# Optimization experiments

Hardware: AMD Instinct MI355X
Metric: run time of the kernel (lower is better)

Reference implementation:

```python
import jax, jax.numpy as jnp
import numpy as np

B = 8192          # number of nodes / batch
DEG = 32          # neighbors per node (fixed-degree instance of the ragged pattern)
E = B * DEG       # total neighbor rows
D = 256           # embedding_dim
A = 128           # attn_dim
ACT = 512         # action_dim
SLOPE = 0.2       # leakyrelu slope


def setup_inputs() -> dict:
    key = jax.random.key(0)
    ks = jax.random.split(key, 12)
    inp = {
        "state": jax.random.normal(ks[0], (B, 2 * D), jnp.float32),
        "now_embedding": jax.random.normal(ks[1], (B, D), jnp.float32),
        "neigh": jax.random.normal(ks[2], (E, D), jnp.float32),
        "seg_ids": jnp.repeat(jnp.arange(B, dtype=jnp.int32), DEG),  # sorted segment ids
        # attention projection Linear(D, A)
        "attn_w": jax.random.normal(ks[3], (D, A), jnp.float32) * (1.0 / np.sqrt(D)),
        "attn_b": jnp.zeros((A,), jnp.float32),
        # attn_weight Linear(2A, 1)
        "aw_w": jax.random.normal(ks[4], (2 * A, 1), jnp.float32) * (1.0 / np.sqrt(2 * A)),
        "aw_b": jnp.zeros((1,), jnp.float32),
        # MLP head
        "w1": jax.random.normal(ks[5], (3 * D, 512), jnp.float32) * (1.0 / np.sqrt(3 * D)),
        "b1": jnp.zeros((512,), jnp.float32),
        "w2": jax.random.normal(ks[6], (512, 1024), jnp.float32) * (1.0 / np.sqrt(512)),
        "b2": jnp.zeros((1024,), jnp.float32),
        "w3": jax.random.normal(ks[7], (1024, ACT), jnp.float32) * (1.0 / np.sqrt(1024)),
        "b3": jnp.zeros((ACT,), jnp.float32),
    }
    return inp


def reference(state, now_embedding, neigh, seg_ids, attn_w, attn_b, aw_w, aw_b,
              w1, b1, w2, b2, w3, b3):
    # project center and neighbor embeddings to attn space
    now_proj = now_embedding @ attn_w + attn_b          # [B, A]
    nb_proj = neigh @ attn_w + attn_b                   # [E, A]
    # attn_weight applied to concat([now_proj[seg], nb_proj]) == split matvec
    w_now, w_nb = aw_w[:A, 0], aw_w[A:, 0]              # [A], [A]
    scores = (now_proj @ w_now)[seg_ids] + nb_proj @ w_nb + aw_b[0]   # [E]
    scores = jnp.where(scores >= 0, scores, SLOPE * scores)           # LeakyReLU(0.2)
    # per-segment (per-node) softmax over neighbors
    seg_max = jax.ops.segment_max(scores, seg_ids, num_segments=B)
    e = jnp.exp(scores - seg_max[seg_ids])
    seg_sum = jax.ops.segment_sum(e, seg_ids, num_segments=B)
    alpha = e / seg_sum[seg_ids]                        # [E]
    # weighted aggregation of raw neighbor embeddings
    agg = jax.ops.segment_sum(alpha[:, None] * neigh, seg_ids, num_segments=B)  # [B, D]
    # MLP head (dropout prob = 0 -> identity)
    out = jnp.concatenate([state, agg], axis=1)         # [B, 3D]
    out = jax.nn.relu(out @ w1 + b1)
    out = jax.nn.relu(out @ w2 + b2)
    out = out @ w3 + b3
    return jax.nn.softmax(out, axis=-1)
```

## Files before the change

kernel.cpp:

```cpp
#include <hip/hip_runtime.h>
#include <hip/hip_bf16.h>

#define B_SEG  8192
#define DEG    32
#define D_DIM  256
#define TWO_D  512
#define ACTD   512
#define SLOPE  0.2f

typedef __attribute__((ext_vector_type(8))) short bf16x8;
typedef __attribute__((ext_vector_type(4))) float f32x4;

#define OFF_VNOW  ((size_t)0)
#define OFF_VNB   ((size_t)1024)
#define OFF_CNST  ((size_t)2048)
#define OFF_W1T   ((size_t)4096)
#define OFF_W2T   (OFF_W1T + (size_t)768*512*2)
#define OFF_W3T   (OFF_W2T + (size_t)512*1024*2)
#define OFF_X1    (OFF_W3T + (size_t)1024*512*2)
#define OFF_X2    (OFF_X1 + (size_t)B_SEG*768*2)
#define OFF_X3    (OFF_X2 + (size_t)B_SEG*512*2)

typedef const unsigned int __attribute__((address_space(1)))* gas_ptr;
typedef unsigned int __attribute__((address_space(3)))* las_ptr;

__device__ __forceinline__ void gload_lds16(const void* g, void* l) {
    __builtin_amdgcn_global_load_lds((gas_ptr)g, (las_ptr)l, 16, 0, 0);
}

__global__ __launch_bounds__(256) void prep_vec(
        const float* __restrict__ attn_w, const float* __restrict__ attn_b,
        const float* __restrict__ aw_w, const float* __restrict__ aw_b,
        float* __restrict__ vnow, float* __restrict__ vnb, float* __restrict__ cnst) {
    const int d = threadIdx.x;
    float s0 = 0.f, s1 = 0.f;
    for (int a = 0; a < 128; ++a) {
        const float w = attn_w[d * 128 + a];
        s0 = fmaf(w, aw_w[a], s0);
        s1 = fmaf(w, aw_w[128 + a], s1);
    }
    vnow[d] = s0;
    vnb[d]  = s1;
    if (d == 0) {
        float c = aw_b[0];
        for (int a = 0; a < 128; ++a) c = fmaf(attn_b[a], aw_w[a] + aw_w[128 + a], c);
        cnst[0] = c;
    }
}

__global__ __launch_bounds__(256) void attn_tr(
        const float* __restrict__ state, const float* __restrict__ now_emb,
        const float* __restrict__ neigh, const float* __restrict__ vnow,
        const float* __restrict__ vnb, const float* __restrict__ cnst,
        __hip_bfloat16* __restrict__ X1,
        const float* __restrict__ w1, const float* __restrict__ w2,
        const float* __restrict__ w3,
        __hip_bfloat16* __restrict__ w1T, __hip_bfloat16* __restrict__ w2T,
        __hip_bfloat16* __restrict__ w3T) {
    __shared__ __align__(16) float smem[1088];
    const int bid = blockIdx.x;

    if (bid >= B_SEG) {
        int pb = bid - B_SEG;
        const float* src;
        __hip_bfloat16* dst;
        int K, N;
        if (pb < 384)      { src = w1; dst = w1T; K = 768;  N = 512;  }
        else if (pb < 896) { pb -= 384; src = w2; dst = w2T; K = 512;  N = 1024; }
        else               { pb -= 896; src = w3; dst = w3T; K = 1024; N = 512;  }
        const int tk = K >> 5;
        const int bk = (pb % tk) * 32;
        const int bn = (pb / tk) * 32;
        float (*tile)[33] = (float(*)[33])smem;
        const int tx = threadIdx.x & 31;
        const int ty = threadIdx.x >> 5;
#pragma unroll
        for (int i = 0; i < 32; i += 8)
            tile[ty + i][tx] = src[(size_t)(bk + ty + i) * N + (bn + tx)];
        __syncthreads();
#pragma unroll
        for (int i = 0; i < 32; i += 8)
            dst[(size_t)(bn + ty + i) * K + (bk + tx)] = __float2bfloat16(tile[tx][ty + i]);
        return;
    }

    const int b    = bid;
    const int tid  = threadIdx.x;
    const int lane = tid & 63;
    const int w    = tid >> 6;
    const int l4   = lane * 4;

    float* s_part  = smem;
    float* s_score = smem + 1024;
    float* s_now   = smem + 1056;

    const float4 vb = *(const float4*)&vnb[l4];
    float4 nv[8];
#pragma unroll
    for (int i = 0; i < 8; ++i) {
        const int e = w * 8 + i;
        nv[i] = *(const float4*)&neigh[((size_t)b * DEG + e) * D_DIM + l4];
        float p = nv[i].x * vb.x + nv[i].y * vb.y + nv[i].z * vb.z + nv[i].w * vb.w;
#pragma unroll
        for (int off = 32; off; off >>= 1) p += __shfl_xor(p, off);
        if (lane == 0) s_score[e] = p;
    }
    if (w == 0) {
        const float4 va = *(const float4*)&vnow[l4];
        const float4 ne = *(const float4*)&now_emb[(size_t)b * D_DIM + l4];
        float p = ne.x * va.x + ne.y * va.y + ne.z * va.z + ne.w * va.w;
#pragma unroll
        for (int off = 32; off; off >>= 1) p += __shfl_xor(p, off);
        if (lane == 0) s_now[0] = p + cnst[0];
    }
    __syncthreads();

    if (w == 0) {
        float s = (lane < DEG) ? (s_score[lane] + s_now[0]) : -3.4e38f;
        s = (s >= 0.f) ? s : SLOPE * s;
        float m = s;
#pragma unroll
        for (int off = 32; off; off >>= 1) m = fmaxf(m, __shfl_xor(m, off));
        const float e = (lane < DEG) ? expf(s - m) : 0.f;
        float t = e;
#pragma unroll
        for (int off = 32; off; off >>= 1) t += __shfl_xor(t, off);
        if (lane < DEG) s_score[lane] = e / t;
    }
    __syncthreads();

    float4 part = {0.f, 0.f, 0.f, 0.f};
#pragma unroll
    for (int i = 0; i < 8; ++i) {
        const float al = s_score[w * 8 + i];
        part.x = fmaf(al, nv[i].x, part.x);
        part.y = fmaf(al, nv[i].y, part.y);
        part.z = fmaf(al, nv[i].z, part.z);
        part.w = fmaf(al, nv[i].w, part.w);
    }
    *(float4*)&s_part[w * D_DIM + l4] = part;
    __syncthreads();

    const float a = s_part[tid] + s_part[D_DIM + tid] + s_part[2 * D_DIM + tid] +
                    s_part[3 * D_DIM + tid];

    __hip_bfloat16* xrow = X1 + (size_t)b * 768;
    xrow[512 + tid] = __float2bfloat16(a);
    const float2 st = *(const float2*)&state[(size_t)b * TWO_D + 2 * tid];
    __hip_bfloat162 h;
    h.x = __float2bfloat16(st.x);
    h.y = __float2bfloat16(st.y);
    *(__hip_bfloat162*)&xrow[2 * tid] = h;
}

template <int RELU, int OUTF32>
__global__ __launch_bounds__(256) void gemm_mfma(
        const __hip_bfloat16* __restrict__ A, const __hip_bfloat16* __restrict__ BT,
        const float* __restrict__ bias, void* __restrict__ Cout, int N, int K) {
    __shared__ __hip_bfloat16 sA[64 * 32];
    __shared__ __hip_bfloat16 sB[128 * 32];

    const int tid  = threadIdx.x;
    const int lane = tid & 63;
    const int wv   = tid >> 6;
    const int wr   = wv >> 1;
    const int wc   = wv & 1;
    const size_t mBase = (size_t)blockIdx.x * 64;
    const size_t nBase = (size_t)blockIdx.y * 128;

    f32x4 acc[2][4];
#pragma unroll
    for (int r = 0; r < 2; ++r)
#pragma unroll
        for (int c = 0; c < 4; ++c) acc[r][c] = (f32x4){0.f, 0.f, 0.f, 0.f};

    const int srow = tid >> 2;
    const int sseg = tid & 3;
    const __hip_bfloat16* gA  = A  + (mBase + srow) * (size_t)K + sseg * 8;
    const __hip_bfloat16* gB0 = BT + (nBase + srow) * (size_t)K + sseg * 8;
    const __hip_bfloat16* gB1 = gB0 + (size_t)64 * K;
    char* ldsA = (char*)&sA[0] + tid * 16;
    char* ldsB = (char*)&sB[0] + tid * 16;

    const int fr  = lane & 15;
    const int fkb = (lane >> 4) * 16;

    for (int k0 = 0; k0 < K; k0 += 32) {
        gload_lds16(gA + k0, ldsA);
        gload_lds16(gB0 + k0, ldsB);
        gload_lds16(gB1 + k0, ldsB + 4096);
        __syncthreads();

        bf16x8 aF[2], bF[4];
#pragma unroll
        for (int r = 0; r < 2; ++r)
            aF[r] = *(const bf16x8*)((const char*)sA + (wr * 32 + r * 16 + fr) * 64 + fkb);
#pragma unroll
        for (int c = 0; c < 4; ++c)
            bF[c] = *(const bf16x8*)((const char*)sB + (wc * 64 + c * 16 + fr) * 64 + fkb);
#pragma unroll
        for (int r = 0; r < 2; ++r)
#pragma unroll
            for (int c = 0; c < 4; ++c)
                acc[r][c] = __builtin_amdgcn_mfma_f32_16x16x32_bf16(aF[r], bF[c], acc[r][c], 0, 0, 0);
        __syncthreads();
    }

    const int fq = lane >> 4;
#pragma unroll
    for (int r = 0; r < 2; ++r) {
#pragma unroll
        for (int c = 0; c < 4; ++c) {
            const size_t col = nBase + wc * 64 + c * 16 + fr;
            const float bcol = bias[col];
#pragma unroll
            for (int q = 0; q < 4; ++q) {
                const size_t row = mBase + wr * 32 + r * 16 + fq * 4 + q;
                float v = acc[r][c][q] + bcol;
                if (RELU) v = fmaxf(v, 0.f);
                if (OUTF32) ((float*)Cout)[row * N + col] = v;
                else ((__hip_bfloat16*)Cout)[row * N + col] = __float2bfloat16(v);
            }
        }
    }
}

__global__ __launch_bounds__(512) void gemm3_softmax(
        const __hip_bfloat16* __restrict__ A, const __hip_bfloat16* __restrict__ BT,
        const float* __restrict__ bias, float* __restrict__ out) {
    constexpr int K = 1024;
    constexpr int N = 512;
    __shared__ __hip_bfloat16 sA[32 * 32];
    __shared__ __hip_bfloat16 sB[512 * 32];
    __shared__ float s_max[8][32];
    __shared__ float s_sum[8][32];
    __shared__ float s_gmax[32];
    __shared__ float s_ginv[32];

    const int tid  = threadIdx.x;
    const int lane = tid & 63;
    const int wv   = tid >> 6;
    const size_t mBase = (size_t)blockIdx.x * 32;

    f32x4 acc[2][4];
#pragma unroll
    for (int r = 0; r < 2; ++r)
#pragma unroll
        for (int c = 0; c < 4; ++c) acc[r][c] = (f32x4){0.f, 0.f, 0.f, 0.f};

    const __hip_bfloat16* gA = A + (mBase + (tid >> 2)) * (size_t)K + (tid & 3) * 8;
    char* ldsA = (char*)&sA[0] + tid * 16;
    const __hip_bfloat16* gB[4];
    char* ldsB[4];
#pragma unroll
    for (int i = 0; i < 4; ++i) {
        const int s = tid + i * 512;
        gB[i]   = BT + (size_t)(s >> 2) * K + (s & 3) * 8;
        ldsB[i] = (char*)&sB[0] + s * 16;
    }

    const int fr  = lane & 15;
    const int fkb = (lane >> 4) * 16;

    for (int k0 = 0; k0 < K; k0 += 32) {
        if (tid < 128) gload_lds16(gA + k0, ldsA);
#pragma unroll
        for (int i = 0; i < 4; ++i) gload_lds16(gB[i] + k0, ldsB[i]);
        __syncthreads();

        bf16x8 aF[2], bF[4];
#pragma unroll
        for (int r = 0; r < 2; ++r)
            aF[r] = *(const bf16x8*)((const char*)sA + (r * 16 + fr) * 64 + fkb);
#pragma unroll
        for (int c = 0; c < 4; ++c)
            bF[c] = *(const bf16x8*)((const char*)sB + (wv * 64 + c * 16 + fr) * 64 + fkb);
#pragma unroll
        for (int r = 0; r < 2; ++r)
#pragma unroll
            for (int c = 0; c < 4; ++c)
                acc[r][c] = __builtin_amdgcn_mfma_f32_16x16x32_bf16(aF[r], bF[c], acc[r][c], 0, 0, 0);
        __syncthreads();
    }

    const int fq = lane >> 4;
    float bcol[4];
#pragma unroll
    for (int c = 0; c < 4; ++c) bcol[c] = bias[wv * 64 + c * 16 + fr];

    float rm[2][4];
#pragma unroll
    for (int r = 0; r < 2; ++r)
#pragma unroll
        for (int q = 0; q < 4; ++q) {
            float m = -3.4e38f;
#pragma unroll
            for (int c = 0; c < 4; ++c) {
                acc[r][c][q] += bcol[c];
                m = fmaxf(m, acc[r][c][q]);
            }
#pragma unroll
            for (int off = 8; off; off >>= 1) m = fmaxf(m, __shfl_xor(m, off));
            rm[r][q] = m;
        }
    if (fr == 0) {
#pragma unroll
        for (int r = 0; r < 2; ++r)
#pragma unroll
            for (int q = 0; q < 4; ++q) s_max[wv][r * 16 + fq * 4 + q] = rm[r][q];
    }
    __syncthreads();
    if (tid < 32) {
        float m = s_max[0][tid];
#pragma unroll
        for (int w2_ = 1; w2_ < 8; ++w2_) m = fmaxf(m, s_max[w2_][tid]);
        s_gmax[tid] = m;
    }
    __syncthreads();

    float rs[2][4];
#pragma unroll
    for (int r = 0; r < 2; ++r)
#pragma unroll
        for (int q = 0; q < 4; ++q) {
            const float gm = s_gmax[r * 16 + fq * 4 + q];
            float s = 0.f;
#pragma unroll
            for (int c = 0; c < 4; ++c) {
                acc[r][c][q] = expf(acc[r][c][q] - gm);
                s += acc[r][c][q];
            }
#pragma unroll
            for (int off = 8; off; off >>= 1) s += __shfl_xor(s, off);
            rs[r][q] = s;
        }
    if (fr == 0) {
#pragma unroll
        for (int r = 0; r < 2; ++r)
#pragma unroll
            for (int q = 0; q < 4; ++q) s_sum[wv][r * 16 + fq * 4 + q] = rs[r][q];
    }
    __syncthreads();
    if (tid < 32) {
        float t = s_sum[0][tid];
#pragma unroll
        for (int w2_ = 1; w2_ < 8; ++w2_) t += s_sum[w2_][tid];
        s_ginv[tid] = 1.f / t;
    }
    __syncthreads();

#pragma unroll
    for (int r = 0; r < 2; ++r)
#pragma unroll
        for (int q = 0; q < 4; ++q) {
            const float inv = s_ginv[r * 16 + fq * 4 + q];
            const size_t row = mBase + r * 16 + fq * 4 + q;
#pragma unroll
            for (int c = 0; c < 4; ++c)
                out[row * N + wv * 64 + c * 16 + fr] = acc[r][c][q] * inv;
        }
}

extern "C" void kernel_launch(void* const* d_in, const int* in_sizes, int n_in,
                              void* d_out, int out_size, void* d_ws, size_t ws_size,
                              hipStream_t stream) {
    const float* state   = (const float*)d_in[0];
    const float* now_emb = (const float*)d_in[1];
    const float* neigh   = (const float*)d_in[2];
    const float* attn_w  = (const float*)d_in[4];
    const float* attn_b  = (const float*)d_in[5];
    const float* aw_w    = (const float*)d_in[6];
    const float* aw_b    = (const float*)d_in[7];
    const float* w1      = (const float*)d_in[8];
    const float* b1      = (const float*)d_in[9];
    const float* w2      = (const float*)d_in[10];
    const float* b2      = (const float*)d_in[11];
    const float* w3      = (const float*)d_in[12];
    const float* b3      = (const float*)d_in[13];
    float* out = (float*)d_out;

    char* ws = (char*)d_ws;
    float*          vnow = (float*)(ws + OFF_VNOW);
    float*          vnb  = (float*)(ws + OFF_VNB);
    float*          cnst = (float*)(ws + OFF_CNST);
    __hip_bfloat16* w1T  = (__hip_bfloat16*)(ws + OFF_W1T);
    __hip_bfloat16* w2T  = (__hip_bfloat16*)(ws + OFF_W2T);
    __hip_bfloat16* w3T  = (__hip_bfloat16*)(ws + OFF_W3T);
    __hip_bfloat16* X1   = (__hip_bfloat16*)(ws + OFF_X1);
    __hip_bfloat16* X2   = (__hip_bfloat16*)(ws + OFF_X2);
    __hip_bfloat16* X3   = (__hip_bfloat16*)(ws + OFF_X3);

    prep_vec<<<1, 256, 0, stream>>>(attn_w, attn_b, aw_w, aw_b, vnow, vnb, cnst);
    attn_tr<<<B_SEG + 1408, 256, 0, stream>>>(state, now_emb, neigh, vnow, vnb, cnst, X1,
                                              w1, w2, w3, w1T, w2T, w3T);
    gemm_mfma<1, 0><<<dim3(128, 4), 256, 0, stream>>>(X1, w1T, b1, (void*)X2, 512, 768);
    gemm_mfma<1, 0><<<dim3(128, 8), 256, 0, stream>>>(X2, w2T, b2, (void*)X3, 1024, 512);
    gemm3_softmax<<<256, 512, 0, stream>>>(X3, w3T, b3, out);
}
```

Before: 149.5 us.

## Double-buffer MLP GEMMs with swizzled LDS and move weight transpose into prep kernel

The two ReLU GEMMs now use a 64-wide K tile with two LDS buffers and an XOR-swizzled layout, so the next tile's global-to-LDS loads are issued while the current tile feeds the MFMAs, and LDS bank conflicts are reduced. The final GEMM+softmax kernel gets the same double buffering. The weight transpose blocks move out of the attention kernel into the prep kernel, which also absorbs the vector precompute, giving attention a simpler launch. The cost is more LDS per block, which may lower occupancy, and the prep kernel's serial block 0 now shares a launch with the transposes.

New measurement: 143.1 us. -4.3%, faster.

```diff
diff --git a/kernel.cpp b/kernel.cpp
--- a/kernel.cpp
+++ b/kernel.cpp
@@ -28,71 +28,68 @@
     __builtin_amdgcn_global_load_lds((gas_ptr)g, (las_ptr)l, 16, 0, 0);
 }
 
-__global__ __launch_bounds__(256) void prep_vec(
+__global__ __launch_bounds__(256) void prep_all(
         const float* __restrict__ attn_w, const float* __restrict__ attn_b,
         const float* __restrict__ aw_w, const float* __restrict__ aw_b,
-        float* __restrict__ vnow, float* __restrict__ vnb, float* __restrict__ cnst) {
-    const int d = threadIdx.x;
-    float s0 = 0.f, s1 = 0.f;
-    for (int a = 0; a < 128; ++a) {
-        const float w = attn_w[d * 128 + a];
-        s0 = fmaf(w, aw_w[a], s0);
-        s1 = fmaf(w, aw_w[128 + a], s1);
-    }
-    vnow[d] = s0;
-    vnb[d]  = s1;
-    if (d == 0) {
-        float c = aw_b[0];
-        for (int a = 0; a < 128; ++a) c = fmaf(attn_b[a], aw_w[a] + aw_w[128 + a], c);
-        cnst[0] = c;
-    }
-}
-
-__global__ __launch_bounds__(256) void attn_tr(
+        const float* __restrict__ w1, const float* __restrict__ w2, const float* __restrict__ w3,
+        float* __restrict__ vnow, float* __restrict__ vnb, float* __restrict__ cnst,
+        __hip_bfloat16* __restrict__ w1T, __hip_bfloat16* __restrict__ w2T,
+        __hip_bfloat16* __restrict__ w3T) {
+    int bid = blockIdx.x;
+    if (bid == 0) {
+        const int d = threadIdx.x;
+        float s0 = 0.f, s1 = 0.f;
+        for (int a = 0; a < 128; ++a) {
+            const float w = attn_w[d * 128 + a];
+            s0 = fmaf(w, aw_w[a], s0);
+            s1 = fmaf(w, aw_w[128 + a], s1);
+        }
+        vnow[d] = s0;
+        vnb[d]  = s1;
+        if (d == 0) {
+            float c = aw_b[0];
+            for (int a = 0; a < 128; ++a) c = fmaf(attn_b[a], aw_w[a] + aw_w[128 + a], c);
+            cnst[0] = c;
+        }
+        return;
+    }
+    bid -= 1;
+    const float* src;
+    __hip_bfloat16* dst;
+    int K, N;
+    if (bid < 384)      { src = w1; dst = w1T; K = 768;  N = 512;  }
+    else if (bid < 896) { bid -= 384; src = w2; dst = w2T; K = 512;  N = 1024; }
+    else                { bid -= 896; src = w3; dst = w3T; K = 1024; N = 512;  }
+    const int tk = K >> 5;
+    const int bk = (bid % tk) * 32;
+    const int bn = (bid / tk) * 32;
+
+    __shared__ float tile[32][33];
+    const int tx = threadIdx.x & 31;
+    const int ty = threadIdx.x >> 5;
+#pragma unroll
+    for (int i = 0; i < 32; i += 8)
+        tile[ty + i][tx] = src[(size_t)(bk + ty + i) * N + (bn + tx)];
+    __syncthreads();
+#pragma unroll
+    for (int i = 0; i < 32; i += 8)
+        dst[(size_t)(bn + ty + i) * K + (bk + tx)] = __float2bfloat16(tile[tx][ty + i]);
+}
+
+__global__ __launch_bounds__(256) void attn_fused(
         const float* __restrict__ state, const float* __restrict__ now_emb,
         const float* __restrict__ neigh, const float* __restrict__ vnow,
         const float* __restrict__ vnb, const float* __restrict__ cnst,
-        __hip_bfloat16* __restrict__ X1,
-        const float* __restrict__ w1, const float* __restrict__ w2,
-        const float* __restrict__ w3,
-        __hip_bfloat16* __restrict__ w1T, __hip_bfloat16* __restrict__ w2T,
-        __hip_bfloat16* __restrict__ w3T) {
-    __shared__ __align__(16) float smem[1088];
-    const int bid = blockIdx.x;
-
-    if (bid >= B_SEG) {
-        int pb = bid - B_SEG;
-        const float* src;
-        __hip_bfloat16* dst;
-        int K, N;
-        if (pb < 384)      { src = w1; dst = w1T; K = 768;  N = 512;  }
-        else if (pb < 896) { pb -= 384; src = w2; dst = w2T; K = 512;  N = 1024; }
-        else               { pb -= 896; src = w3; dst = w3T; K = 1024; N = 512;  }
-        const int tk = K >> 5;
-        const int bk = (pb % tk) * 32;
-        const int bn = (pb / tk) * 32;
-        float (*tile)[33] = (float(*)[33])smem;
-        const int tx = threadIdx.x & 31;
-        const int ty = threadIdx.x >> 5;
-#pragma unroll
-        for (int i = 0; i < 32; i += 8)
-            tile[ty + i][tx] = src[(size_t)(bk + ty + i) * N + (bn + tx)];
-        __syncthreads();
-#pragma unroll
-        for (int i = 0; i < 32; i += 8)
-            dst[(size_t)(bn + ty + i) * K + (bk + tx)] = __float2bfloat16(tile[tx][ty + i]);
-        return;
-    }
-
-    const int b    = bid;
+        __hip_bfloat16* __restrict__ X1) {
+    const int b    = blockIdx.x;
     const int tid  = threadIdx.x;
     const int lane = tid & 63;
     const int w    = tid >> 6;
     const int l4   = lane * 4;
 
-    float* s_part  = smem;
-    float* s_score = smem + 1024;
-    float* s_now   = smem + 1056;
+    __shared__ float s_score[DEG];
+    __shared__ float s_now;
+    __shared__ float s_part[4][D_DIM];
 
     const float4 vb = *(const float4*)&vnb[l4];
     float4 nv[8];
@@ -111,12 +108,12 @@
         float p = ne.x * va.x + ne.y * va.y + ne.z * va.z + ne.w * va.w;
 #pragma unroll
         for (int off = 32; off; off >>= 1) p += __shfl_xor(p, off);
-        if (lane == 0) s_now[0] = p + cnst[0];
+        if (lane == 0) s_now = p + cnst[0];
     }
     __syncthreads();
 
     if (w == 0) {
-        float s = (lane < DEG) ? (s_score[lane] + s_now[0]) : -3.4e38f;
+        float s = (lane < DEG) ? (s_score[lane] + s_now) : -3.4e38f;
         s = (s >= 0.f) ? s : SLOPE * s;
         float m = s;
 #pragma unroll
@@ -138,11 +135,10 @@
         part.z = fmaf(al, nv[i].z, part.z);
         part.w = fmaf(al, nv[i].w, part.w);
     }
-    *(float4*)&s_part[w * D_DIM + l4] = part;
-    __syncthreads();
-
-    const float a = s_part[tid] + s_part[D_DIM + tid] + s_part[2 * D_DIM + tid] +
-                    s_part[3 * D_DIM + tid];
+    *(float4*)&s_part[w][l4] = part;
+    __syncthreads();
+
+    const float a = s_part[0][tid] + s_part[1][tid] + s_part[2][tid] + s_part[3][tid];
 
     __hip_bfloat16* xrow = X1 + (size_t)b * 768;
     xrow[512 + tid] = __float2bfloat16(a);
@@ -154,11 +150,11 @@
 }
 
 template <int RELU, int OUTF32>
-__global__ __launch_bounds__(256) void gemm_mfma(
+__global__ __launch_bounds__(256) void gemm_db(
         const __hip_bfloat16* __restrict__ A, const __hip_bfloat16* __restrict__ BT,
         const float* __restrict__ bias, void* __restrict__ Cout, int N, int K) {
-    __shared__ __hip_bfloat16 sA[64 * 32];
-    __shared__ __hip_bfloat16 sB[128 * 32];
+    __shared__ __hip_bfloat16 sA[2][64 * 64];
+    __shared__ __hip_bfloat16 sB[2][128 * 64];
 
     const int tid  = threadIdx.x;
     const int lane = tid & 63;
@@ -167,6 +163,7 @@
     const int wc   = wv & 1;
     const size_t mBase = (size_t)blockIdx.x * 64;
     const size_t nBase = (size_t)blockIdx.y * 128;
+    const size_t Kb = (size_t)K * 2;
 
     f32x4 acc[2][4];
 #pragma unroll
@@ -174,37 +171,65 @@
 #pragma unroll
         for (int c = 0; c < 4; ++c) acc[r][c] = (f32x4){0.f, 0.f, 0.f, 0.f};
 
-    const int srow = tid >> 2;
-    const int sseg = tid & 3;
-    const __hip_bfloat16* gA  = A  + (mBase + srow) * (size_t)K + sseg * 8;
-    const __hip_bfloat16* gB0 = BT + (nBase + srow) * (size_t)K + sseg * 8;
-    const __hip_bfloat16* gB1 = gB0 + (size_t)64 * K;
-    char* ldsA = (char*)&sA[0] + tid * 16;
-    char* ldsB = (char*)&sB[0] + tid * 16;
+    const int srow  = tid >> 3;
+    const int kbLog = ((tid & 7) ^ (srow & 7)) << 4;
+    const char* gA = (const char*)A  + (mBase + srow) * Kb + kbLog;
+    const char* gB = (const char*)BT + (nBase + srow) * Kb + kbLog;
+    char* lA = (char*)&sA[0][0] + tid * 16;
+    char* lB = (char*)&sB[0][0] + tid * 16;
 
     const int fr  = lane & 15;
     const int fkb = (lane >> 4) * 16;
-
-    for (int k0 = 0; k0 < K; k0 += 32) {
-        gload_lds16(gA + k0, ldsA);
-        gload_lds16(gB0 + k0, ldsB);
-        gload_lds16(gB1 + k0, ldsB + 4096);
+    const char* sAb = (const char*)&sA[0][0];
+    const char* sBb = (const char*)&sB[0][0];
+
+    const int nk = K >> 6;
+
+#define STAGE(T, BUF) do {                                                         \
+        const size_t kOff = (size_t)(T) * 128;                                     \
+        gload_lds16(gA + kOff,           lA + (BUF) * 8192);                       \
+        gload_lds16(gA + kOff + 32 * Kb, lA + (BUF) * 8192 + 4096);                \
+        gload_lds16(gB + kOff,           lB + (BUF) * 16384);                      \
+        gload_lds16(gB + kOff + 32 * Kb, lB + (BUF) * 16384 + 4096);               \
+        gload_lds16(gB + kOff + 64 * Kb, lB + (BUF) * 16384 + 8192);               \
+        gload_lds16(gB + kOff + 96 * Kb, lB + (BUF) * 16384 + 12288);              \
+    } while (0)
+
+#define SWZ(ROW, KB) ((ROW) * 128 + ((KB) ^ (((ROW) & 7) << 4)))
+
+    STAGE(0, 0);
+    __syncthreads();
+
+    int cur = 0;
+    for (int t = 0; t < nk; ++t) {
+        if (t + 1 < nk) STAGE(t + 1, cur ^ 1);
+
+        const char* bufA = sAb + cur * 8192;
+        const char* bufB = sBb + cur * 16384;
+#pragma unroll
+        for (int ks = 0; ks < 2; ++ks) {
+            bf16x8 aF[2], bF[4];
+#pragma unroll
+            for (int r = 0; r < 2; ++r) {
+                const int row = wr * 32 + r * 16 + fr;
+                aF[r] = *(const bf16x8*)(bufA + SWZ(row, ks * 64 + fkb));
+            }
+#pragma unroll
+            for (int c = 0; c < 4; ++c) {
+                const int row = wc * 64 + c * 16 + fr;
+                bF[c] = *(const bf16x8*)(bufB + SWZ(row, ks * 64 + fkb));
+            }
+#pragma unroll
+            for (int r = 0; r < 2; ++r)
+#pragma unroll
+                for (int c = 0; c < 4; ++c)
+                    acc[r][c] = __builtin_amdgcn_mfma_f32_16x16x32_bf16(aF[r], bF[c], acc[r][c], 0, 0, 0);
+        }
         __syncthreads();
-
-        bf16x8 aF[2], bF[4];
-#pragma unroll
-        for (int r = 0; r < 2; ++r)
-            aF[r] = *(const bf16x8*)((const char*)sA + (wr * 32 + r * 16 + fr) * 64 + fkb);
-#pragma unroll
-        for (int c = 0; c < 4; ++c)
-            bF[c] = *(const bf16x8*)((const char*)sB + (wc * 64 + c * 16 + fr) * 64 + fkb);
-#pragma unroll
-        for (int r = 0; r < 2; ++r)
-#pragma unroll
-            for (int c = 0; c < 4; ++c)
-                acc[r][c] = __builtin_amdgcn_mfma_f32_16x16x32_bf16(aF[r], bF[c], acc[r][c], 0, 0, 0);
-        __syncthreads();
-    }
+        cur ^= 1;
+    }
+#undef STAGE
+#undef SWZ
 
     const int fq = lane >> 4;
 #pragma unroll
@@ -230,8 +255,8 @@
         const float* __restrict__ bias, float* __restrict__ out) {
     constexpr int K = 1024;
     constexpr int N = 512;
-    __shared__ __hip_bfloat16 sA[32 * 32];
-    __shared__ __hip_bfloat16 sB[512 * 32];
+    __shared__ __hip_bfloat16 sA[2][32 * 32];
+    __shared__ __hip_bfloat16 sB[2][512 * 32];
     __shared__ float s_max[8][32];
     __shared__ float s_sum[8][32];
     __shared__ float s_gmax[32];
@@ -249,39 +274,51 @@
         for (int c = 0; c < 4; ++c) acc[r][c] = (f32x4){0.f, 0.f, 0.f, 0.f};
 
     const __hip_bfloat16* gA = A + (mBase + (tid >> 2)) * (size_t)K + (tid & 3) * 8;
-    char* ldsA = (char*)&sA[0] + tid * 16;
+    char* lA = (char*)&sA[0][0] + tid * 16;
     const __hip_bfloat16* gB[4];
-    char* ldsB[4];
+    char* lB[4];
 #pragma unroll
     for (int i = 0; i < 4; ++i) {
         const int s = tid + i * 512;
-        gB[i]   = BT + (size_t)(s >> 2) * K + (s & 3) * 8;
-        ldsB[i] = (char*)&sB[0] + s * 16;
+        gB[i] = BT + (size_t)(s >> 2) * K + (s & 3) * 8;
+        lB[i] = (char*)&sB[0][0] + s * 16;
     }
 
     const int fr  = lane & 15;
     const int fkb = (lane >> 4) * 16;
 
-    for (int k0 = 0; k0 < K; k0 += 32) {
-        if (tid < 128) gload_lds16(gA + k0, ldsA);
-#pragma unroll
-        for (int i = 0; i < 4; ++i) gload_lds16(gB[i] + k0, ldsB[i]);
-        __syncthreads();
-
+#define STAGE3(T, BUF) do {                                                        \
+        const int kOff = (T) * 32;                                                 \
+        if (tid < 128) gload_lds16(gA + kOff, lA + (BUF) * 2048);                  \
+        _Pragma("unroll")                                                          \
+        for (int i = 0; i < 4; ++i) gload_lds16(gB[i] + kOff, lB[i] + (BUF) * 32768); \
+    } while (0)
+
+    STAGE3(0, 0);
+    __syncthreads();
+
+    int cur = 0;
+    for (int t = 0; t < 32; ++t) {
+        if (t + 1 < 32) STAGE3(t + 1, cur ^ 1);
+
+        const char* bufA = (const char*)&sA[cur][0];
+        const char* bufB = (const char*)&sB[cur][0];
         bf16x8 aF[2], bF[4];
 #pragma unroll
         for (int r = 0; r < 2; ++r)
-            aF[r] = *(const bf16x8*)((const char*)sA + (r * 16 + fr) * 64 + fkb);
+            aF[r] = *(const bf16x8*)(bufA + (r * 16 + fr) * 64 + fkb);
 #pragma unroll
         for (int c = 0; c < 4; ++c)
-            bF[c] = *(const bf16x8*)((const char*)sB + (wv * 64 + c * 16 + fr) * 64 + fkb);
+            bF[c] = *(const bf16x8*)(bufB + (wv * 64 + c * 16 + fr) * 64 + fkb);
 #pragma unroll
         for (int r = 0; r < 2; ++r)
 #pragma unroll
             for (int c = 0; c < 4; ++c)
                 acc[r][c] = __builtin_amdgcn_mfma_f32_16x16x32_bf16(aF[r], bF[c], acc[r][c], 0, 0, 0);
         __syncthreads();
-    }
+        cur ^= 1;
+    }
+#undef STAGE3
 
     const int fq = lane >> 4;
     float bcol[4];
@@ -390,10 +427,10 @@
     __hip_bfloat16* X2   = (__hip_bfloat16*)(ws + OFF_X2);
     __hip_bfloat16* X3   = (__hip_bfloat16*)(ws + OFF_X3);
 
-    prep_vec<<<1, 256, 0, stream>>>(attn_w, attn_b, aw_w, aw_b, vnow, vnb, cnst);
-    attn_tr<<<B_SEG + 1408, 256, 0, stream>>>(state, now_emb, neigh, vnow, vnb, cnst, X1,
-                                              w1, w2, w3, w1T, w2T, w3T);
-    gemm_mfma<1, 0><<<dim3(128, 4), 256, 0, stream>>>(X1, w1T, b1, (void*)X2, 512, 768);
-    gemm_mfma<1, 0><<<dim3(128, 8), 256, 0, stream>>>(X2, w2T, b2, (void*)X3, 1024, 512);
+    prep_all<<<1409, 256, 0, stream>>>(attn_w, attn_b, aw_w, aw_b, w1, w2, w3,
+                                       vnow, vnb, cnst, w1T, w2T, w3T);
+    attn_fused<<<B_SEG, 256, 0, stream>>>(state, now_emb, neigh, vnow, vnb, cnst, X1);
+    gemm_db<1, 0><<<dim3(128, 4), 256, 0, stream>>>(X1, w1T, b1, (void*)X2, 512, 768);
+    gemm_db<1, 0><<<dim3(128, 8), 256, 0, stream>>>(X2, w2T, b2, (void*)X3, 1024, 512);
     gemm3_softmax<<<256, 512, 0, stream>>>(X3, w3T, b3, out);
 }
```
